# Kernel optimization log

Hardware: AMD Instinct MI355X
Metric: run time of the kernel (lower is better)

Reference implementation:

```python
import jax, jax.numpy as jnp
import numpy as np

N_NODES = 100000
N_EDGES = 1600000
D = 128          # in = hidden = out channels
N_LAYERS = 3


def setup_inputs() -> dict:
    key = jax.random.key(0)
    ks = jax.random.split(key, 20)
    inp = {
        "x": jax.random.normal(ks[0], (N_NODES, D), jnp.float32),
        "edge_index": jax.random.randint(ks[1], (2, N_EDGES), 0, N_NODES, dtype=jnp.int64),
    }
    s = 1.0 / np.sqrt(D)
    k = 2
    for l in range(N_LAYERS):
        inp[f"w1_{l}"] = jax.random.normal(ks[k], (D, D), jnp.float32) * s; k += 1
        inp[f"b1_{l}"] = jnp.zeros((D,), jnp.float32)
        inp[f"w2_{l}"] = jax.random.normal(ks[k], (D, D), jnp.float32) * s; k += 1
        inp[f"b2_{l}"] = jnp.zeros((D,), jnp.float32)
    # JK concat: 3 layers * D channels -> out D
    inp["jk_w"] = jax.random.normal(ks[k], (N_LAYERS * D, D), jnp.float32) * (1.0 / np.sqrt(N_LAYERS * D))
    inp["jk_b"] = jnp.zeros((D,), jnp.float32)
    return inp


def _gin_layer(x, src, dst, w1, b1, w2, b2):
    # GINConv, eps=0: h = (1+eps)*x + sum_{j in N(i)} x_j ; then MLP Lin-ReLU-Lin
    agg = jax.ops.segment_sum(x[src], dst, num_segments=N_NODES)  # [N, D]
    h = x + agg
    h = jax.nn.relu(h @ w1 + b1)
    return h @ w2 + b2


def reference(x, edge_index, w1_0, b1_0, w2_0, b2_0, w1_1, b1_1, w2_1, b2_1,
              w1_2, b1_2, w2_2, b2_2, jk_w, jk_b):
    src, dst = edge_index[0], edge_index[1]
    layers = [(w1_0, b1_0, w2_0, b2_0), (w1_1, b1_1, w2_1, b2_1), (w1_2, b1_2, w2_2, b2_2)]
    xs = []
    for i, (w1, b1, w2, b2) in enumerate(layers):
        # dropout is identity in eval mode
        residual = x  # skip_proj is Identity since in==out channels
        x = _gin_layer(x, src, dst, w1, b1, w2, b2) + residual
        if i != N_LAYERS - 1:
            x = jax.nn.elu(x)
        xs.append(x)
    x = jnp.concatenate(xs, axis=-1)  # JK 'cat' -> [N, 3*D]
    return x @ jk_w + jk_b
```

## Files before the change

### kernel.cpp

```cpp
#include <hip/hip_runtime.h>

typedef __bf16 bf16x8 __attribute__((ext_vector_type(8)));
typedef float f32x4 __attribute__((ext_vector_type(4)));

#define CHUNK 4096
#define NBUCK 512

struct WPack { const float* p[9]; };

__device__ inline __bf16 f2bf(float f){ return (__bf16)f; }

__global__ __launch_bounds__(256) void prep_kernel(WPack pk, __bf16* __restrict__ wf,
    const float* __restrict__ x, __bf16* __restrict__ xb, int n8){
  int b = blockIdx.x, t = threadIdx.x;
  if (b < 576){
    int tid = b*256 + t;
    int m = tid >> 14;
    int r = tid & 16383;
    int j = r & 7;
    int lane = (r >> 3) & 63;
    int ks = (r >> 9) & 3;
    int c = r >> 11;
    int k = ks*32 + ((lane>>4)<<3) + j;
    int col = (c<<4) + (lane & 15);
    wf[tid] = f2bf(pk.p[m][k*128 + col]);
  } else {
    int i = (b - 576)*256 + t;
    if (i >= n8) return;
    f32x4 a = ((const f32x4*)x)[2*i];
    f32x4 bb = ((const f32x4*)x)[2*i+1];
    bf16x8 r;
    r[0]=f2bf(a[0]); r[1]=f2bf(a[1]); r[2]=f2bf(a[2]); r[3]=f2bf(a[3]);
    r[4]=f2bf(bb[0]); r[5]=f2bf(bb[1]); r[6]=f2bf(bb[2]); r[7]=f2bf(bb[3]);
    ((bf16x8*)xb)[i] = r;
  }
}

__global__ __launch_bounds__(256) void p1_count(const int* __restrict__ ei, int E, int NBLK,
    int* __restrict__ cnt){
  __shared__ int h[NBUCK];
  int b = blockIdx.x, t = threadIdx.x;
  h[t] = 0; h[t + 256] = 0;
  __syncthreads();
  int base = b*CHUNK;
  int lim = E - base; if (lim > CHUNK) lim = CHUNK;
  for (int i = t; i < lim; i += 256)
    atomicAdd(&h[ei[E + base + i] >> 8], 1);
  __syncthreads();
  cnt[t*NBLK + b] = h[t];
  cnt[(t + 256)*NBLK + b] = h[t + 256];
}

__global__ __launch_bounds__(256) void scan1_kernel(const int* __restrict__ cnt, int* __restrict__ bsum, int L){
  __shared__ int sh[256];
  int b = blockIdx.x, t = threadIdx.x;
  int base = b*2048 + t*8;
  int s = 0;
  #pragma unroll
  for (int j = 0; j < 8; j++){ int i = base + j; if (i < L) s += cnt[i]; }
  sh[t] = s; __syncthreads();
  for (int off = 128; off > 0; off >>= 1){
    if (t < off) sh[t] += sh[t + off];
    __syncthreads();
  }
  if (t == 0) bsum[b] = sh[0];
}

__global__ __launch_bounds__(256) void scan2_kernel(const int* __restrict__ bsum, int* __restrict__ boff,
                                                    int NB, int* __restrict__ total_out){
  __shared__ int sh[256];
  int t = threadIdx.x;
  int v = (t < NB) ? bsum[t] : 0;
  sh[t] = v; __syncthreads();
  for (int off = 1; off < 256; off <<= 1){
    int u = (t >= off) ? sh[t - off] : 0;
    __syncthreads();
    sh[t] += u;
    __syncthreads();
  }
  if (t < NB) boff[t] = sh[t] - v;
  if (t == 255) *total_out = sh[255];
}

__global__ __launch_bounds__(256) void scan3_kernel(const int* __restrict__ cnt, const int* __restrict__ boff,
                                                    int* __restrict__ off, int L){
  __shared__ int sh[256];
  int b = blockIdx.x, t = threadIdx.x;
  int base = b*2048 + t*8;
  int loc[8]; int s = 0;
  #pragma unroll
  for (int j = 0; j < 8; j++){ int i = base + j; int d = (i < L) ? cnt[i] : 0; loc[j] = d; s += d; }
  sh[t] = s; __syncthreads();
  for (int o = 1; o < 256; o <<= 1){
    int u = (t >= o) ? sh[t - o] : 0;
    __syncthreads();
    sh[t] += u;
    __syncthreads();
  }
  int excl = boff[b] + sh[t] - s;
  #pragma unroll
  for (int j = 0; j < 8; j++){ int i = base + j; if (i < L) off[i] = excl; excl += loc[j]; }
}

__global__ __launch_bounds__(256) void p3_scatter(const int* __restrict__ ei, int E, int NBLK,
    const int* __restrict__ off, int* __restrict__ tpack){
  __shared__ int cur[NBUCK];
  int b = blockIdx.x, t = threadIdx.x;
  cur[t]       = off[t*NBLK + b];
  cur[t + 256] = off[(t + 256)*NBLK + b];
  __syncthreads();
  int base = b*CHUNK;
  int lim = E - base; if (lim > CHUNK) lim = CHUNK;
  for (int i = t; i < lim; i += 256){
    int s = ei[base + i];
    int d = ei[E + base + i];
    int p = atomicAdd(&cur[d >> 8], 1);
    tpack[p] = (s << 8) | (d & 255);
  }
}

__global__ __launch_bounds__(256) void p4_build(const int* __restrict__ tpack,
    const int* __restrict__ off, int NBLK, int E, int N,
    int* __restrict__ rs, int* __restrict__ csr){
  __shared__ int dc[256], sc[256];
  int q = blockIdx.x, t = threadIdx.x;
  int bstart = off[q*NBLK];
  int bend = (q == NBUCK-1) ? E : off[(q+1)*NBLK];
  dc[t] = 0;
  __syncthreads();
  for (int i = bstart + t; i < bend; i += 256)
    atomicAdd(&dc[tpack[i] & 255], 1);
  __syncthreads();
  int v = dc[t];
  sc[t] = v; __syncthreads();
  for (int o = 1; o < 256; o <<= 1){
    int u = (t >= o) ? sc[t - o] : 0;
    __syncthreads();
    sc[t] += u;
    __syncthreads();
  }
  int ex = sc[t] - v;
  int gd = q*256 + t;
  if (gd < N) rs[gd] = bstart + ex;
  __syncthreads();
  dc[t] = ex;
  __syncthreads();
  for (int i = bstart + t; i < bend; i += 256){
    int p = tpack[i];
    int r = atomicAdd(&dc[p & 255], 1);
    csr[bstart + r] = p >> 8;
  }
}

__global__ __launch_bounds__(256) void agg_kernel(const __bf16* __restrict__ xb,
    const int* __restrict__ rs, const int* __restrict__ csr,
    __bf16* __restrict__ hb, int N)
{
  int node = blockIdx.x*4 + (threadIdx.x >> 6);
  if (node >= N) return;
  int lane = threadIdx.x & 63;
  int quad = lane >> 4;
  int l16  = lane & 15;
  int s = rs[node], e = rs[node+1];
  float a[8] = {0.f,0.f,0.f,0.f,0.f,0.f,0.f,0.f};
  for (int base = s; base < e; base += 64){
    int idx = base + lane;
    int nb = (idx < e) ? csr[idx] : 0;
    int cnt = e - base; if (cnt > 64) cnt = 64;
    int t = 0;
    #pragma unroll 2
    for (; t + 8 <= cnt; t += 8){
      int sA = __shfl(nb, t + quad);
      int sB = __shfl(nb, t + 4 + quad);
      bf16x8 vA = ((const bf16x8*)(xb + (long)sA*128))[l16];
      bf16x8 vB = ((const bf16x8*)(xb + (long)sB*128))[l16];
      #pragma unroll
      for (int j = 0; j < 8; j++) a[j] += (float)vA[j] + (float)vB[j];
    }
    for (; t < cnt; t += 4){
      int i = t + quad;
      int ic = (i < cnt) ? i : (cnt - 1);
      int sA = __shfl(nb, ic);
      bf16x8 vA = ((const bf16x8*)(xb + (long)sA*128))[l16];
      if (i < cnt){
        #pragma unroll
        for (int j = 0; j < 8; j++) a[j] += (float)vA[j];
      }
    }
  }
  if (quad == 0){
    bf16x8 sv = ((const bf16x8*)(xb + (long)node*128))[l16];
    #pragma unroll
    for (int j = 0; j < 8; j++) a[j] += (float)sv[j];
  }
  #pragma unroll
  for (int j = 0; j < 8; j++){
    a[j] += __shfl_xor(a[j], 16);
    a[j] += __shfl_xor(a[j], 32);
  }
  if (quad == 0){
    bf16x8 r;
    #pragma unroll
    for (int j = 0; j < 8; j++) r[j] = f2bf(a[j]);
    ((bf16x8*)(hb + (long)node*128))[l16] = r;
  }
}

template<int ACT2>
__global__ __launch_bounds__(256) void fused_mlp(const __bf16* __restrict__ A,
    const __bf16* __restrict__ wf1, const __bf16* __restrict__ wf2,
    const float* __restrict__ b1, const float* __restrict__ b2,
    const __bf16* __restrict__ res, __bf16* __restrict__ out, int M)
{
  __shared__ __bf16 H[128][136];
  int lane = threadIdx.x & 63;
  int wid = threadIdx.x >> 6;
  long row0 = (long)blockIdx.x * 128;
  const bf16x8* w1v = (const bf16x8*)wf1;
  const bf16x8* w2v = (const bf16x8*)wf2;
  bf16x8 bv1[2][4], bv2[2][4];
  #pragma unroll
  for (int c2 = 0; c2 < 2; c2++)
    #pragma unroll
    for (int ks = 0; ks < 4; ks++){
      bv1[c2][ks] = w1v[((wid*2 + c2)*4 + ks)*64 + lane];
      bv2[c2][ks] = w2v[((wid*2 + c2)*4 + ks)*64 + lane];
    }
  int col0 = wid*32 + (lane & 15);
  float bb1_0 = b1[col0], bb1_1 = b1[col0 + 16];
  float bb2_0 = b2[col0], bb2_1 = b2[col0 + 16];
  int koff = (lane >> 4) << 3;
  #pragma unroll 2
  for (int rt = 0; rt < 8; rt++){
    long row = row0 + rt*16 + (lane & 15);
    long rowc = (row < M) ? row : (long)(M-1);
    const __bf16* ap = A + rowc*128 + koff;
    bf16x8 av[4];
    #pragma unroll
    for (int ks = 0; ks < 4; ks++)
      av[ks] = *(const bf16x8*)(ap + ks*32);
    f32x4 acc0 = {0.f,0.f,0.f,0.f}, acc1 = {0.f,0.f,0.f,0.f};
    #pragma unroll
    for (int ks = 0; ks < 4; ks++){
      acc0 = __builtin_amdgcn_mfma_f32_16x16x32_bf16(av[ks], bv1[0][ks], acc0, 0, 0, 0);
      acc1 = __builtin_amdgcn_mfma_f32_16x16x32_bf16(av[ks], bv1[1][ks], acc1, 0, 0, 0);
    }
    int r0 = rt*16 + ((lane >> 4) << 2);
    #pragma unroll
    for (int c2 = 0; c2 < 2; c2++){
      f32x4 acc = c2 ? acc1 : acc0;
      int col = col0 + c2*16;
      float bb = c2 ? bb1_1 : bb1_0;
      #pragma unroll
      for (int i = 0; i < 4; i++)
        H[r0 + i][col] = f2bf(fmaxf(acc[i] + bb, 0.f));
    }
  }
  __syncthreads();
  #pragma unroll 2
  for (int rt = 0; rt < 8; rt++){
    int r = rt*16 + (lane & 15);
    bf16x8 av[4];
    #pragma unroll
    for (int ks = 0; ks < 4; ks++)
      av[ks] = *(const bf16x8*)(&H[r][ks*32 + koff]);
    f32x4 acc0 = {0.f,0.f,0.f,0.f}, acc1 = {0.f,0.f,0.f,0.f};
    #pragma unroll
    for (int ks = 0; ks < 4; ks++){
      acc0 = __builtin_amdgcn_mfma_f32_16x16x32_bf16(av[ks], bv2[0][ks], acc0, 0, 0, 0);
      acc1 = __builtin_amdgcn_mfma_f32_16x16x32_bf16(av[ks], bv2[1][ks], acc1, 0, 0, 0);
    }
    long orow0 = row0 + rt*16 + ((lane >> 4) << 2);
    #pragma unroll
    for (int c2 = 0; c2 < 2; c2++){
      f32x4 acc = c2 ? acc1 : acc0;
      int col = col0 + c2*16;
      float bb = c2 ? bb2_1 : bb2_0;
      #pragma unroll
      for (int i = 0; i < 4; i++){
        long orow = orow0 + i;
        if (orow < M){
          long idx = orow*128 + col;
          float v = acc[i] + bb + (float)res[idx];
          if (ACT2 == 2) v = (v > 0.f) ? v : (__expf(v) - 1.f);
          out[idx] = f2bf(v);
        }
      }
    }
  }
}

__global__ __launch_bounds__(256) void fused_mlp_jk(const __bf16* __restrict__ A,
    const __bf16* __restrict__ y1g, const __bf16* __restrict__ y2g,
    const __bf16* __restrict__ wf1, const __bf16* __restrict__ wf2,
    const __bf16* __restrict__ wfjk,
    const float* __restrict__ b1, const float* __restrict__ b2,
    const float* __restrict__ jkb, float* __restrict__ out, int M)
{
  __shared__ __bf16 H[128][136];
  __shared__ __bf16 Y3[128][136];
  int lane = threadIdx.x & 63;
  int wid = threadIdx.x >> 6;
  long row0 = (long)blockIdx.x * 128;
  const bf16x8* w1v = (const bf16x8*)wf1;
  const bf16x8* w2v = (const bf16x8*)wf2;
  bf16x8 bv1[2][4], bv2[2][4];
  #pragma unroll
  for (int c2 = 0; c2 < 2; c2++)
    #pragma unroll
    for (int ks = 0; ks < 4; ks++){
      bv1[c2][ks] = w1v[((wid*2 + c2)*4 + ks)*64 + lane];
      bv2[c2][ks] = w2v[((wid*2 + c2)*4 + ks)*64 + lane];
    }
  int col0 = wid*32 + (lane & 15);
  float bb1_0 = b1[col0], bb1_1 = b1[col0 + 16];
  float bb2_0 = b2[col0], bb2_1 = b2[col0 + 16];
  int koff = (lane >> 4) << 3;
  #pragma unroll 2
  for (int rt = 0; rt < 8; rt++){
    long row = row0 + rt*16 + (lane & 15);
    long rowc = (row < M) ? row : (long)(M-1);
    const __bf16* ap = A + rowc*128 + koff;
    bf16x8 av[4];
    #pragma unroll
    for (int ks = 0; ks < 4; ks++)
      av[ks] = *(const bf16x8*)(ap + ks*32);
    f32x4 acc0 = {0.f,0.f,0.f,0.f}, acc1 = {0.f,0.f,0.f,0.f};
    #pragma unroll
    for (int ks = 0; ks < 4; ks++){
      acc0 = __builtin_amdgcn_mfma_f32_16x16x32_bf16(av[ks], bv1[0][ks], acc0, 0, 0, 0);
      acc1 = __builtin_amdgcn_mfma_f32_16x16x32_bf16(av[ks], bv1[1][ks], acc1, 0, 0, 0);
    }
    int r0 = rt*16 + ((lane >> 4) << 2);
    #pragma unroll
    for (int c2 = 0; c2 < 2; c2++){
      f32x4 acc = c2 ? acc1 : acc0;
      int col = col0 + c2*16;
      float bb = c2 ? bb1_1 : bb1_0;
      #pragma unroll
      for (int i = 0; i < 4; i++)
        H[r0 + i][col] = f2bf(fmaxf(acc[i] + bb, 0.f));
    }
  }
  __syncthreads();
  #pragma unroll 2
  for (int rt = 0; rt < 8; rt++){
    int r = rt*16 + (lane & 15);
    bf16x8 av[4];
    #pragma unroll
    for (int ks = 0; ks < 4; ks++)
      av[ks] = *(const bf16x8*)(&H[r][ks*32 + koff]);
    f32x4 acc0 = {0.f,0.f,0.f,0.f}, acc1 = {0.f,0.f,0.f,0.f};
    #pragma unroll
    for (int ks = 0; ks < 4; ks++){
      acc0 = __builtin_amdgcn_mfma_f32_16x16x32_bf16(av[ks], bv2[0][ks], acc0, 0, 0, 0);
      acc1 = __builtin_amdgcn_mfma_f32_16x16x32_bf16(av[ks], bv2[1][ks], acc1, 0, 0, 0);
    }
    long orow0 = row0 + rt*16 + ((lane >> 4) << 2);
    int r0 = rt*16 + ((lane >> 4) << 2);
    #pragma unroll
    for (int c2 = 0; c2 < 2; c2++){
      f32x4 acc = c2 ? acc1 : acc0;
      int col = col0 + c2*16;
      float bb = c2 ? bb2_1 : bb2_0;
      #pragma unroll
      for (int i = 0; i < 4; i++){
        long orow = orow0 + i;
        float rv = (orow < M) ? (float)y2g[orow*128 + col] : 0.f;
        Y3[r0 + i][col] = f2bf(acc[i] + bb + rv);
      }
    }
  }
  __syncthreads();
  const bf16x8* wjv = (const bf16x8*)wfjk;
  bf16x8 bvj[2][12];
  #pragma unroll
  for (int c2 = 0; c2 < 2; c2++)
    #pragma unroll
    for (int ks = 0; ks < 12; ks++)
      bvj[c2][ks] = wjv[(size_t)(ks>>2)*2048 + (size_t)((wid*2 + c2)*4 + (ks&3))*64 + lane];
  float jb0 = jkb[col0], jb1 = jkb[col0 + 16];
  #pragma unroll 1
  for (int rt = 0; rt < 8; rt++){
    long row = row0 + rt*16 + (lane & 15);
    long rowc = (row < M) ? row : (long)(M-1);
    int rl = rt*16 + (lane & 15);
    f32x4 acc0 = {0.f,0.f,0.f,0.f}, acc1 = {0.f,0.f,0.f,0.f};
    #pragma unroll
    for (int ks = 0; ks < 12; ks++){
      bf16x8 av;
      if (ks < 4)      av = *(const bf16x8*)(y1g + rowc*128 + ks*32 + koff);
      else if (ks < 8) av = *(const bf16x8*)(y2g + rowc*128 + (ks-4)*32 + koff);
      else             av = *(const bf16x8*)(&Y3[rl][(ks-8)*32 + koff]);
      acc0 = __builtin_amdgcn_mfma_f32_16x16x32_bf16(av, bvj[0][ks], acc0, 0, 0, 0);
      acc1 = __builtin_amdgcn_mfma_f32_16x16x32_bf16(av, bvj[1][ks], acc1, 0, 0, 0);
    }
    long orow0 = row0 + rt*16 + ((lane >> 4) << 2);
    #pragma unroll
    for (int c2 = 0; c2 < 2; c2++){
      f32x4 acc = c2 ? acc1 : acc0;
      int col = col0 + c2*16;
      float bb = c2 ? jb1 : jb0;
      #pragma unroll
      for (int i = 0; i < 4; i++){
        long orow = orow0 + i;
        if (orow < M)
          out[orow*128 + col] = acc[i] + bb;
      }
    }
  }
}

extern "C" void kernel_launch(void* const* d_in, const int* in_sizes, int n_in,
                              void* d_out, int out_size, void* d_ws, size_t ws_size,
                              hipStream_t stream)
{
  const float* x   = (const float*)d_in[0];
  const int*   ei  = (const int*)d_in[1];
  const float* w1[3] = {(const float*)d_in[2], (const float*)d_in[6], (const float*)d_in[10]};
  const float* b1[3] = {(const float*)d_in[3], (const float*)d_in[7], (const float*)d_in[11]};
  const float* w2[3] = {(const float*)d_in[4], (const float*)d_in[8], (const float*)d_in[12]};
  const float* b2[3] = {(const float*)d_in[5], (const float*)d_in[9], (const float*)d_in[13]};
  const float* jkw = (const float*)d_in[14];
  const float* jkb = (const float*)d_in[15];
  int N = in_sizes[0] / 128;
  int E = in_sizes[1] / 2;
  float* outp = (float*)d_out;

  char* wptr = (char*)d_ws;
  auto alloc = [&](size_t bytes)->void*{
    void* p = (void*)wptr; wptr += (bytes + 255) & ~(size_t)255; return p;
  };
  int NBLK = (E + CHUNK - 1) / CHUNK;
  int L = NBUCK * NBLK;
  int* rs    = (int*)alloc((size_t)(N+1)*4);
  int* csr   = (int*)alloc((size_t)E*4);
  int* tpack = (int*)alloc((size_t)E*4);
  int* cnt   = (int*)alloc((size_t)L*4);
  int* off   = (int*)alloc((size_t)L*4);
  __bf16* y[3];
  for (int i = 0; i < 3; i++) y[i] = (__bf16*)alloc((size_t)N*128*2);
  __bf16* hb = (__bf16*)alloc((size_t)N*128*2);
  __bf16* wf = (__bf16*)alloc((size_t)9*16384*2);
  int nsb = (L + 2047) / 2048;
  int* bsum = (int*)alloc((size_t)nsb*4);
  int* boff = (int*)alloc((size_t)nsb*4);

  WPack pk;
  pk.p[0] = w1[0]; pk.p[1] = w2[0];
  pk.p[2] = w1[1]; pk.p[3] = w2[1];
  pk.p[4] = w1[2]; pk.p[5] = w2[2];
  pk.p[6] = jkw; pk.p[7] = jkw + 16384; pk.p[8] = jkw + 32768;
  int n8 = N*128/8;
  prep_kernel<<<576 + (n8 + 255)/256, 256, 0, stream>>>(pk, wf, x, y[0], n8);

  p1_count<<<NBLK, 256, 0, stream>>>(ei, E, NBLK, cnt);
  scan1_kernel<<<nsb, 256, 0, stream>>>(cnt, bsum, L);
  scan2_kernel<<<1, 256, 0, stream>>>(bsum, boff, nsb, rs + N);
  scan3_kernel<<<nsb, 256, 0, stream>>>(cnt, boff, off, L);
  p3_scatter<<<NBLK, 256, 0, stream>>>(ei, E, NBLK, off, tpack);
  p4_build<<<NBUCK, 256, 0, stream>>>(tpack, off, NBLK, E, N, rs, csr);

  int gemm_blocks = (N + 127)/128;
  for (int l = 0; l < 3; l++){
    agg_kernel<<<(N + 3)/4, 256, 0, stream>>>(y[l], rs, csr, hb, N);
    if (l < 2)
      fused_mlp<2><<<gemm_blocks, 256, 0, stream>>>(hb, wf + (size_t)(2*l)*16384, wf + (size_t)(2*l+1)*16384,
                                                    b1[l], b2[l], y[l], y[l+1], N);
    else
      fused_mlp_jk<<<gemm_blocks, 256, 0, stream>>>(hb, y[1], y[2],
                                                    wf + (size_t)4*16384, wf + (size_t)5*16384, wf + (size_t)6*16384,
                                                    b1[2], b2[2], jkb, outp, N);
  }
}
```

Measured before the change: 404.0 us.

## Swizzle shared MLP tile, reuse one LDS buffer, restructure JK GEMM for occupancy

The padded shared-memory tiles are replaced with an unpadded 128x128 bf16 buffer that uses an XOR swizzle to avoid bank conflicts. The JK kernel now reuses that one buffer for the layer-3 output instead of allocating a second tile, with an extra barrier before overwriting it. The JK GEMM loop is restructured to load one 128-column weight slice at a time over half-tiles, replacing the 24 resident weight vectors. Together with launch_bounds(256,4), this aims to cut LDS and register use so more blocks fit per CU, at the cost of reloading weight slices and adding a sync per row tile.

```diff
diff --git a/kernel.cpp b/kernel.cpp
--- a/kernel.cpp
+++ b/kernel.cpp
@@ -9,6 +9,13 @@
 struct WPack { const float* p[9]; };
 
 __device__ inline __bf16 f2bf(float f){ return (__bf16)f; }
+
+__device__ inline int hswz(int r, int c){
+  return (r << 7) + ((((c >> 3) ^ (r & 7)) << 3) | (c & 7));
+}
+__device__ inline const __bf16* hvec(const __bf16* H, int r, int g){
+  return H + (r << 7) + (((g ^ (r & 7)) & 15) << 3);
+}
 
 __global__ __launch_bounds__(256) void prep_kernel(WPack pk, __bf16* __restrict__ wf,
     const float* __restrict__ x, __bf16* __restrict__ xb, int n8){
@@ -207,14 +214,15 @@
 }
 
 template<int ACT2>
-__global__ __launch_bounds__(256) void fused_mlp(const __bf16* __restrict__ A,
+__global__ __launch_bounds__(256, 4) void fused_mlp(const __bf16* __restrict__ A,
     const __bf16* __restrict__ wf1, const __bf16* __restrict__ wf2,
     const float* __restrict__ b1, const float* __restrict__ b2,
     const __bf16* __restrict__ res, __bf16* __restrict__ out, int M)
 {
-  __shared__ __bf16 H[128][136];
+  __shared__ __bf16 H[128*128];
   int lane = threadIdx.x & 63;
   int wid = threadIdx.x >> 6;
+  int quad = lane >> 4;
   long row0 = (long)blockIdx.x * 128;
   const bf16x8* w1v = (const bf16x8*)wf1;
   const bf16x8* w2v = (const bf16x8*)wf2;
@@ -229,7 +237,7 @@
   int col0 = wid*32 + (lane & 15);
   float bb1_0 = b1[col0], bb1_1 = b1[col0 + 16];
   float bb2_0 = b2[col0], bb2_1 = b2[col0 + 16];
-  int koff = (lane >> 4) << 3;
+  int koff = quad << 3;
   #pragma unroll 2
   for (int rt = 0; rt < 8; rt++){
     long row = row0 + rt*16 + (lane & 15);
@@ -245,7 +253,7 @@
       acc0 = __builtin_amdgcn_mfma_f32_16x16x32_bf16(av[ks], bv1[0][ks], acc0, 0, 0, 0);
       acc1 = __builtin_amdgcn_mfma_f32_16x16x32_bf16(av[ks], bv1[1][ks], acc1, 0, 0, 0);
     }
-    int r0 = rt*16 + ((lane >> 4) << 2);
+    int r0 = rt*16 + (quad << 2);
     #pragma unroll
     for (int c2 = 0; c2 < 2; c2++){
       f32x4 acc = c2 ? acc1 : acc0;
@@ -253,7 +261,7 @@
       float bb = c2 ? bb1_1 : bb1_0;
       #pragma unroll
       for (int i = 0; i < 4; i++)
-        H[r0 + i][col] = f2bf(fmaxf(acc[i] + bb, 0.f));
+        H[hswz(r0 + i, col)] = f2bf(fmaxf(acc[i] + bb, 0.f));
     }
   }
   __syncthreads();
@@ -263,14 +271,14 @@
     bf16x8 av[4];
     #pragma unroll
     for (int ks = 0; ks < 4; ks++)
-      av[ks] = *(const bf16x8*)(&H[r][ks*32 + koff]);
+      av[ks] = *(const bf16x8*)hvec(H, r, 4*ks + quad);
     f32x4 acc0 = {0.f,0.f,0.f,0.f}, acc1 = {0.f,0.f,0.f,0.f};
     #pragma unroll
     for (int ks = 0; ks < 4; ks++){
       acc0 = __builtin_amdgcn_mfma_f32_16x16x32_bf16(av[ks], bv2[0][ks], acc0, 0, 0, 0);
       acc1 = __builtin_amdgcn_mfma_f32_16x16x32_bf16(av[ks], bv2[1][ks], acc1, 0, 0, 0);
     }
-    long orow0 = row0 + rt*16 + ((lane >> 4) << 2);
+    long orow0 = row0 + rt*16 + (quad << 2);
     #pragma unroll
     for (int c2 = 0; c2 < 2; c2++){
       f32x4 acc = c2 ? acc1 : acc0;
@@ -290,17 +298,17 @@
   }
 }
 
-__global__ __launch_bounds__(256) void fused_mlp_jk(const __bf16* __restrict__ A,
+__global__ __launch_bounds__(256, 4) void fused_mlp_jk(const __bf16* __restrict__ A,
     const __bf16* __restrict__ y1g, const __bf16* __restrict__ y2g,
     const __bf16* __restrict__ wf1, const __bf16* __restrict__ wf2,
     const __bf16* __restrict__ wfjk,
     const float* __restrict__ b1, const float* __restrict__ b2,
     const float* __restrict__ jkb, float* __restrict__ out, int M)
 {
-  __shared__ __bf16 H[128][136];
-  __shared__ __bf16 Y3[128][136];
+  __shared__ __bf16 H[128*128];
   int lane = threadIdx.x & 63;
   int wid = threadIdx.x >> 6;
+  int quad = lane >> 4;
   long row0 = (long)blockIdx.x * 128;
   const bf16x8* w1v = (const bf16x8*)wf1;
   const bf16x8* w2v = (const bf16x8*)wf2;
@@ -315,7 +323,7 @@
   int col0 = wid*32 + (lane & 15);
   float bb1_0 = b1[col0], bb1_1 = b1[col0 + 16];
   float bb2_0 = b2[col0], bb2_1 = b2[col0 + 16];
-  int koff = (lane >> 4) << 3;
+  int koff = quad << 3;
   #pragma unroll 2
   for (int rt = 0; rt < 8; rt++){
     long row = row0 + rt*16 + (lane & 15);
@@ -331,7 +339,7 @@
       acc0 = __builtin_amdgcn_mfma_f32_16x16x32_bf16(av[ks], bv1[0][ks], acc0, 0, 0, 0);
       acc1 = __builtin_amdgcn_mfma_f32_16x16x32_bf16(av[ks], bv1[1][ks], acc1, 0, 0, 0);
     }
-    int r0 = rt*16 + ((lane >> 4) << 2);
+    int r0 = rt*16 + (quad << 2);
     #pragma unroll
     for (int c2 = 0; c2 < 2; c2++){
       f32x4 acc = c2 ? acc1 : acc0;
@@ -339,73 +347,116 @@
       float bb = c2 ? bb1_1 : bb1_0;
       #pragma unroll
       for (int i = 0; i < 4; i++)
-        H[r0 + i][col] = f2bf(fmaxf(acc[i] + bb, 0.f));
-    }
-  }
-  __syncthreads();
-  #pragma unroll 2
+        H[hswz(r0 + i, col)] = f2bf(fmaxf(acc[i] + bb, 0.f));
+    }
+  }
+  __syncthreads();
+  #pragma unroll 1
   for (int rt = 0; rt < 8; rt++){
     int r = rt*16 + (lane & 15);
     bf16x8 av[4];
     #pragma unroll
     for (int ks = 0; ks < 4; ks++)
-      av[ks] = *(const bf16x8*)(&H[r][ks*32 + koff]);
+      av[ks] = *(const bf16x8*)hvec(H, r, 4*ks + quad);
     f32x4 acc0 = {0.f,0.f,0.f,0.f}, acc1 = {0.f,0.f,0.f,0.f};
     #pragma unroll
     for (int ks = 0; ks < 4; ks++){
       acc0 = __builtin_amdgcn_mfma_f32_16x16x32_bf16(av[ks], bv2[0][ks], acc0, 0, 0, 0);
       acc1 = __builtin_amdgcn_mfma_f32_16x16x32_bf16(av[ks], bv2[1][ks], acc1, 0, 0, 0);
     }
-    long orow0 = row0 + rt*16 + ((lane >> 4) << 2);
-    int r0 = rt*16 + ((lane >> 4) << 2);
+    long orow0 = row0 + rt*16 + (quad << 2);
+    int r0 = rt*16 + (quad << 2);
+    float rv[2][4];
+    #pragma unroll
+    for (int c2 = 0; c2 < 2; c2++)
+      #pragma unroll
+      for (int i = 0; i < 4; i++){
+        long orow = orow0 + i;
+        rv[c2][i] = (orow < M) ? (float)y2g[orow*128 + col0 + c2*16] : 0.f;
+      }
+    __syncthreads();
     #pragma unroll
     for (int c2 = 0; c2 < 2; c2++){
       f32x4 acc = c2 ? acc1 : acc0;
       int col = col0 + c2*16;
       float bb = c2 ? bb2_1 : bb2_0;
       #pragma unroll
-      for (int i = 0; i < 4; i++){
-        long orow = orow0 + i;
-        float rv = (orow < M) ? (float)y2g[orow*128 + col] : 0.f;
-        Y3[r0 + i][col] = f2bf(acc[i] + bb + rv);
-      }
+      for (int i = 0; i < 4; i++)
+        H[hswz(r0 + i, col)] = f2bf(acc[i] + bb + rv[c2][i]);
     }
   }
   __syncthreads();
   const bf16x8* wjv = (const bf16x8*)wfjk;
-  bf16x8 bvj[2][12];
-  #pragma unroll
-  for (int c2 = 0; c2 < 2; c2++)
-    #pragma unroll
-    for (int ks = 0; ks < 12; ks++)
-      bvj[c2][ks] = wjv[(size_t)(ks>>2)*2048 + (size_t)((wid*2 + c2)*4 + (ks&3))*64 + lane];
   float jb0 = jkb[col0], jb1 = jkb[col0 + 16];
   #pragma unroll 1
-  for (int rt = 0; rt < 8; rt++){
-    long row = row0 + rt*16 + (lane & 15);
-    long rowc = (row < M) ? row : (long)(M-1);
-    int rl = rt*16 + (lane & 15);
-    f32x4 acc0 = {0.f,0.f,0.f,0.f}, acc1 = {0.f,0.f,0.f,0.f};
-    #pragma unroll
-    for (int ks = 0; ks < 12; ks++){
-      bf16x8 av;
-      if (ks < 4)      av = *(const bf16x8*)(y1g + rowc*128 + ks*32 + koff);
-      else if (ks < 8) av = *(const bf16x8*)(y2g + rowc*128 + (ks-4)*32 + koff);
-      else             av = *(const bf16x8*)(&Y3[rl][(ks-8)*32 + koff]);
-      acc0 = __builtin_amdgcn_mfma_f32_16x16x32_bf16(av, bvj[0][ks], acc0, 0, 0, 0);
-      acc1 = __builtin_amdgcn_mfma_f32_16x16x32_bf16(av, bvj[1][ks], acc1, 0, 0, 0);
-    }
-    long orow0 = row0 + rt*16 + ((lane >> 4) << 2);
-    #pragma unroll
-    for (int c2 = 0; c2 < 2; c2++){
-      f32x4 acc = c2 ? acc1 : acc0;
-      int col = col0 + c2*16;
-      float bb = c2 ? jb1 : jb0;
-      #pragma unroll
-      for (int i = 0; i < 4; i++){
-        long orow = orow0 + i;
-        if (orow < M)
-          out[orow*128 + col] = acc[i] + bb;
+  for (int half = 0; half < 2; half++){
+    f32x4 acc[4][2];
+    #pragma unroll
+    for (int q = 0; q < 4; q++){
+      acc[q][0] = (f32x4){jb0, jb0, jb0, jb0};
+      acc[q][1] = (f32x4){jb1, jb1, jb1, jb1};
+    }
+    #pragma unroll 1
+    for (int src = 0; src < 2; src++){
+      const __bf16* yg = src ? y2g : y1g;
+      bf16x8 bv[2][4];
+      #pragma unroll
+      for (int c2 = 0; c2 < 2; c2++)
+        #pragma unroll
+        for (int ks = 0; ks < 4; ks++)
+          bv[c2][ks] = wjv[(size_t)src*2048 + (size_t)((wid*2 + c2)*4 + ks)*64 + lane];
+      #pragma unroll
+      for (int q = 0; q < 4; q++){
+        int rt = half*4 + q;
+        long row = row0 + rt*16 + (lane & 15);
+        long rowc = (row < M) ? row : (long)(M-1);
+        const __bf16* ap = yg + rowc*128 + koff;
+        bf16x8 av[4];
+        #pragma unroll
+        for (int ks = 0; ks < 4; ks++)
+          av[ks] = *(const bf16x8*)(ap + ks*32);
+        #pragma unroll
+        for (int ks = 0; ks < 4; ks++){
+          acc[q][0] = __builtin_amdgcn_mfma_f32_16x16x32_bf16(av[ks], bv[0][ks], acc[q][0], 0, 0, 0);
+          acc[q][1] = __builtin_amdgcn_mfma_f32_16x16x32_bf16(av[ks], bv[1][ks], acc[q][1], 0, 0, 0);
+        }
+      }
+    }
+    {
+      bf16x8 bv[2][4];
+      #pragma unroll
+      for (int c2 = 0; c2 < 2; c2++)
+        #pragma unroll
+        for (int ks = 0; ks < 4; ks++)
+          bv[c2][ks] = wjv[(size_t)2*2048 + (size_t)((wid*2 + c2)*4 + ks)*64 + lane];
+      #pragma unroll
+      for (int q = 0; q < 4; q++){
+        int rt = half*4 + q;
+        int r = rt*16 + (lane & 15);
+        bf16x8 av[4];
+        #pragma unroll
+        for (int ks = 0; ks < 4; ks++)
+          av[ks] = *(const bf16x8*)hvec(H, r, 4*ks + quad);
+        #pragma unroll
+        for (int ks = 0; ks < 4; ks++){
+          acc[q][0] = __builtin_amdgcn_mfma_f32_16x16x32_bf16(av[ks], bv[0][ks], acc[q][0], 0, 0, 0);
+          acc[q][1] = __builtin_amdgcn_mfma_f32_16x16x32_bf16(av[ks], bv[1][ks], acc[q][1], 0, 0, 0);
+        }
+      }
+    }
+    #pragma unroll
+    for (int q = 0; q < 4; q++){
+      int rt = half*4 + q;
+      long orow0 = row0 + rt*16 + (quad << 2);
+      #pragma unroll
+      for (int c2 = 0; c2 < 2; c2++){
+        int col = col0 + c2*16;
+        #pragma unroll
+        for (int i = 0; i < 4; i++){
+          long orow = orow0 + i;
+          if (orow < M)
+            out[orow*128 + col] = acc[q][c2][i];
+        }
       }
     }
   }
```

Measured after the change: 391.9 us. -3.0%, faster.
